# Kernel optimization log

Hardware: AMD Instinct MI355X
Metric: run time of the kernel (lower is better)

The kernel has to match this reference:

```python
import jax, jax.numpy as jnp
import numpy as np

B, INDIM, ENC, BOT, DEC = 2048, 20000, 512, 128, 512
EPS = 1e-5


def _bn(x, g, b):
    # BatchNorm1d in training mode: biased batch stats
    m = jnp.mean(x, axis=0)
    v = jnp.mean(jnp.square(x - m), axis=0)
    return (x - m) * jax.lax.rsqrt(v + EPS) * g + b


def setup_inputs() -> dict:
    key = jax.random.key(0)
    ks = jax.random.split(key, 8)
    s = 0.02  # small init scale keeps exp() outputs finite
    return {
        "x": jax.random.uniform(ks[0], (B, INDIM), dtype=jnp.float32),
        "bn0_g": jnp.ones((INDIM,), jnp.float32),
        "bn0_b": jnp.zeros((INDIM,), jnp.float32),
        "enc_W": jax.random.normal(ks[1], (ENC, INDIM), jnp.float32) * s,
        "enc_b": jnp.zeros((ENC,), jnp.float32),
        "bn1_g": jnp.ones((ENC,), jnp.float32),
        "bn1_b": jnp.zeros((ENC,), jnp.float32),
        "bot_W": jax.random.normal(ks[2], (BOT, ENC), jnp.float32) * s,
        "bot_b": jnp.zeros((BOT,), jnp.float32),
        "bn2_g": jnp.ones((BOT,), jnp.float32),
        "bn2_b": jnp.zeros((BOT,), jnp.float32),
        "dec_W": jax.random.normal(ks[3], (DEC, BOT), jnp.float32) * s,
        "dec_b": jnp.zeros((DEC,), jnp.float32),
        "o1_W": jax.random.normal(ks[4], (INDIM, DEC), jnp.float32) * s,
        "o1_b": jnp.zeros((INDIM,), jnp.float32),
        "o2_W": jax.random.normal(ks[5], (INDIM, DEC), jnp.float32) * s,
        "o2_b": jnp.zeros((INDIM,), jnp.float32),
        "o3_W": jax.random.normal(ks[6], (INDIM, DEC), jnp.float32) * s,
        "o3_b": jnp.zeros((INDIM,), jnp.float32),
    }


def reference(x, bn0_g, bn0_b, enc_W, enc_b, bn1_g, bn1_b, bot_W, bot_b,
              bn2_g, bn2_b, dec_W, dec_b, o1_W, o1_b, o2_W, o2_b, o3_W, o3_b):
    # row-sum / median normalization; diag-inverse @ x == x / s[:, None]
    row_sum = jnp.sum(x, axis=1)                     # [B]
    s = row_sum / jnp.median(row_sum)                # [B]
    h = jnp.log1p(x / s[:, None])                    # log(inv(diag(s)) @ x + 1)
    h = _bn(h, bn0_g, bn0_b)
    h = jax.nn.relu(h @ enc_W.T + enc_b)
    h = _bn(h, bn1_g, bn1_b)
    h = jax.nn.relu(h @ bot_W.T + bot_b)
    h = _bn(h, bn2_g, bn2_b)
    h = jax.nn.relu(h @ dec_W.T + dec_b)
    M = jnp.exp(h @ o1_W.T + o1_b)
    M_loss = s[:, None] * M                          # diag(s) @ M
    pai = jax.nn.sigmoid(h @ o2_W.T + o2_b)
    theta = jnp.exp(h @ o3_W.T + o3_b)
    return pai, M, theta, M_loss
```

## Files before the change

### kernel.cpp

```cpp
#include <hip/hip_runtime.h>
#include <hip/hip_bf16.h>
#include <math.h>

#define B_    2048
#define IND   20000
#define ENCN  512
#define BOTN  128
#define DECN  512
#define KP1   20480
#define NP    20224
#define SPLITK 16
#define KSTEP1 20
#define SPLITK2 4
#define BNEPS 1e-5f

typedef __hip_bfloat16 bf16;
typedef __bf16 bf16x8 __attribute__((ext_vector_type(8)));
typedef float f32x4 __attribute__((ext_vector_type(4)));
typedef unsigned short u16;

__device__ __forceinline__ u16 f2bfu(float f) {
  __hip_bfloat16 h = __float2bfloat16(f);
  return *reinterpret_cast<u16*>(&h);
}

__device__ __forceinline__ void st_b64_bf16(void* p, f32x4 v) {
  union { u16 u[4]; uint2 d; } o;
  o.u[0] = f2bfu(v[0]); o.u[1] = f2bfu(v[1]);
  o.u[2] = f2bfu(v[2]); o.u[3] = f2bfu(v[3]);
  *(uint2*)p = o.d;
}

__device__ __forceinline__ void gload_lds16(const bf16* g, bf16* l) {
  __builtin_amdgcn_global_load_lds(
      (const __attribute__((address_space(1))) void*)g,
      (__attribute__((address_space(3))) void*)l, 16, 0, 0);
}

__global__ void rowsum_k(const float* __restrict__ x, float* __restrict__ row_sum) {
  const int row = blockIdx.x;
  const f32x4* xr = (const f32x4*)(x + (size_t)row * IND);
  float s = 0.f;
  for (int i = threadIdx.x; i < IND / 4; i += 256) {
    f32x4 v = xr[i];
    s += (v[0] + v[1]) + (v[2] + v[3]);
  }
#pragma unroll
  for (int o = 32; o > 0; o >>= 1) s += __shfl_down(s, o, 64);
  __shared__ float ws4[4];
  if ((threadIdx.x & 63) == 0) ws4[threadIdx.x >> 6] = s;
  __syncthreads();
  if (threadIdx.x == 0) row_sum[row] = (ws4[0] + ws4[1]) + (ws4[2] + ws4[3]);
}

__global__ void median_scale_k(const float* __restrict__ row_sum,
                               float* __restrict__ sArr, float* __restrict__ invs) {
  __shared__ float v[B_];
  const int tid = threadIdx.x;
  v[tid] = row_sum[tid];
  v[tid + 1024] = row_sum[tid + 1024];
  __syncthreads();
  for (int k = 2; k <= B_; k <<= 1) {
    for (int j = k >> 1; j > 0; j >>= 1) {
      for (int i = tid; i < B_; i += 1024) {
        int ixj = i ^ j;
        if (ixj > i) {
          bool up = ((i & k) == 0);
          float a = v[i], b = v[ixj];
          if ((a > b) == up) { v[i] = b; v[ixj] = a; }
        }
      }
      __syncthreads();
    }
  }
  float med = 0.5f * (v[B_ / 2 - 1] + v[B_ / 2]);
  for (int i = tid; i < B_; i += 1024) {
    float rs = row_sum[i];
    sArr[i] = rs / med;
    invs[i] = med / rs;
  }
}

__global__ void pass2_k(const float* __restrict__ x, const float* __restrict__ invs,
                        bf16* __restrict__ L, float* __restrict__ part_s,
                        float* __restrict__ part_q) {
  const int c0 = (blockIdx.x * 256 + threadIdx.x) * 4;
  const int rblk = blockIdx.y;
  const int r0 = rblk * 32;
  const bool valid = (c0 < IND);
  f32x4 sum = {0.f, 0.f, 0.f, 0.f}, sq = {0.f, 0.f, 0.f, 0.f};
  for (int r = r0; r < r0 + 32; ++r) {
    f32x4 lv = {0.f, 0.f, 0.f, 0.f};
    if (valid) {
      f32x4 v = *(const f32x4*)(x + (size_t)r * IND + c0);
      float iv = invs[r];
      lv[0] = log1pf(v[0] * iv); lv[1] = log1pf(v[1] * iv);
      lv[2] = log1pf(v[2] * iv); lv[3] = log1pf(v[3] * iv);
      sum += lv; sq += lv * lv;
    }
    ushort4 o;
    o.x = f2bfu(lv[0]); o.y = f2bfu(lv[1]); o.z = f2bfu(lv[2]); o.w = f2bfu(lv[3]);
    *(ushort4*)((u16*)L + (size_t)r * KP1 + c0) = o;
  }
  if (valid) {
    *(f32x4*)(part_s + (size_t)rblk * KP1 + c0) = sum;
    *(f32x4*)(part_q + (size_t)rblk * KP1 + c0) = sq;
  }
}

__global__ void finalize_bn_k(const float* __restrict__ part_s, const float* __restrict__ part_q,
                              const float* __restrict__ g, const float* __restrict__ b,
                              float* __restrict__ scale, float* __restrict__ shift) {
  int c = blockIdx.x * 256 + threadIdx.x;
  if (c >= IND) return;
  float s = 0.f, q = 0.f;
  for (int z = 0; z < 64; ++z) {
    s += part_s[(size_t)z * KP1 + c];
    q += part_q[(size_t)z * KP1 + c];
  }
  const float invN = 1.f / (float)B_;
  float mean = s * invN;
  float var = q * invN - mean * mean;
  float sc = g[c] * rsqrtf(var + BNEPS);
  scale[c] = sc;
  shift[c] = b[c] - mean * sc;
}

__global__ void prepw_k(const float* __restrict__ encW, const float* __restrict__ enc_b,
                        const float* __restrict__ scale0, const float* __restrict__ shift0,
                        bf16* __restrict__ Wp, float* __restrict__ bias1) {
  const int e = blockIdx.x;
  float local = 0.f;
  for (int j0 = threadIdx.x * 4; j0 < KP1; j0 += 1024) {
    ushort4 o;
    if (j0 < IND) {
      f32x4 w = *(const f32x4*)(encW + (size_t)e * IND + j0);
      f32x4 sc = *(const f32x4*)(scale0 + j0);
      f32x4 sh = *(const f32x4*)(shift0 + j0);
      local += sh[0] * w[0] + sh[1] * w[1] + sh[2] * w[2] + sh[3] * w[3];
      o.x = f2bfu(w[0] * sc[0]); o.y = f2bfu(w[1] * sc[1]);
      o.z = f2bfu(w[2] * sc[2]); o.w = f2bfu(w[3] * sc[3]);
    } else {
      o.x = 0; o.y = 0; o.z = 0; o.w = 0;
    }
    *(ushort4*)((u16*)Wp + (size_t)e * KP1 + j0) = o;
  }
#pragma unroll
  for (int o = 32; o > 0; o >>= 1) local += __shfl_down(local, o, 64);
  __shared__ float red[4];
  if ((threadIdx.x & 63) == 0) red[threadIdx.x >> 6] = local;
  __syncthreads();
  if (threadIdx.x == 0) bias1[e] = enc_b[e] + ((red[0] + red[1]) + (red[2] + red[3]));
}

__global__ __launch_bounds__(512, 2)
void gemm1_k(const bf16* __restrict__ A, const bf16* __restrict__ Bm,
             float* __restrict__ Cp) {
  extern __shared__ __align__(16) bf16 smem[];
  bf16* AsB = smem;
  bf16* BsB = smem + 32768;
  const int tid = threadIdx.x;
  const int lane = tid & 63;
  const int wave = tid >> 6;
  const int wr = wave >> 2;
  const int wc = wave & 3;

  const int bid = blockIdx.x;
  const int swz = (bid & 7) * 32 + (bid >> 3);
  const int xm = swz & 7;
  const int rest = swz >> 3;
  const int yn = rest & 1;
  const int z = rest >> 1;
  const int m0 = xm * 256;
  const int n0 = yn * 256;
  const int kbeg = z * KSTEP1 * 64;

  const int srow = tid >> 3;
  const int schunk = (tid & 7) ^ (srow & 7);
  const bf16* gA = A + (size_t)(m0 + srow) * KP1 + kbeg + schunk * 8;
  const bf16* gB = Bm + (size_t)(n0 + srow) * KP1 + kbeg + schunk * 8;
  const int ldst = tid * 8;

  f32x4 acc[8][4] = {};
  const int lrow = lane & 15;
  const int kq = lane >> 4;

  auto STAGE = [&](int ks, int buf) {
    const bf16* ga = gA + (size_t)ks * 64;
    const bf16* gb = gB + (size_t)ks * 64;
    bf16* la = AsB + buf * 16384 + ldst;
    bf16* lb = BsB + buf * 16384 + ldst;
#pragma unroll
    for (int i = 0; i < 4; ++i) {
      gload_lds16(ga + (size_t)(i * 64) * KP1, la + i * 4096);
      gload_lds16(gb + (size_t)(i * 64) * KP1, lb + i * 4096);
    }
  };

  STAGE(0, 0);
  asm volatile("s_waitcnt vmcnt(0)" ::: "memory");
  __builtin_amdgcn_s_barrier();

  int cur = 0;
  for (int ks = 0; ks < KSTEP1; ++ks) {
    if (ks + 1 < KSTEP1) STAGE(ks + 1, cur ^ 1);
    const bf16* As = AsB + cur * 16384;
    const bf16* Bs = BsB + cur * 16384;
#pragma unroll
    for (int kk = 0; kk < 2; ++kk) {
      const int kc = kk * 4 + kq;
      bf16x8 af[8], bfv[4];
#pragma unroll
      for (int m = 0; m < 8; ++m) {
        const int row = wr * 128 + m * 16 + lrow;
        af[m] = *(const bf16x8*)(&As[row * 64 + ((kc ^ (row & 7)) << 3)]);
      }
#pragma unroll
      for (int n = 0; n < 4; ++n) {
        const int row = wc * 64 + n * 16 + lrow;
        bfv[n] = *(const bf16x8*)(&Bs[row * 64 + ((kc ^ (row & 7)) << 3)]);
      }
#pragma unroll
      for (int m = 0; m < 8; ++m)
#pragma unroll
        for (int n = 0; n < 4; ++n)
          acc[m][n] = __builtin_amdgcn_mfma_f32_16x16x32_bf16(bfv[n], af[m], acc[m][n], 0, 0, 0);
    }
    if (ks + 1 < KSTEP1) {
      asm volatile("s_waitcnt vmcnt(0)" ::: "memory");
      __builtin_amdgcn_s_barrier();
      cur ^= 1;
    }
  }

  float* o0 = Cp + (size_t)z * ((size_t)B_ * ENCN);
  const int growb = m0 + wr * 128 + lrow;
  const int gcolb = n0 + wc * 64 + kq * 4;
#pragma unroll
  for (int m = 0; m < 8; ++m) {
    const int grow = growb + m * 16;
#pragma unroll
    for (int n = 0; n < 4; ++n) {
      const int gcol = gcolb + n * 16;
      *(f32x4*)(&o0[(size_t)grow * ENCN + gcol]) = acc[m][n];
    }
  }
}

__global__ __launch_bounds__(512, 2)
void gemm_out_k(const bf16* __restrict__ h3,
                const float* __restrict__ W0, const float* __restrict__ W1,
                const float* __restrict__ W2,
                const float* __restrict__ b0, const float* __restrict__ b1,
                const float* __restrict__ b2,
                const float* __restrict__ sArr, float* __restrict__ out) {
  extern __shared__ __align__(16) bf16 smem[];
  bf16* AsB = smem;
  bf16* BsB = smem + 32768;
  const int tid = threadIdx.x;
  const int lane = tid & 63;
  const int wave = tid >> 6;
  const int wr = wave >> 2;
  const int wc = wave & 3;

  const int bid = blockIdx.x;
  const int swz = (bid & 7) * 237 + (bid >> 3);
  const int g = swz / 632;
  const int r2 = swz - g * 632;
  const int xm = r2 & 7;
  const int yn = r2 >> 3;
  const int m0 = xm * 256;
  const int n0 = yn * 256;

  const float* Wg = (g == 0) ? W0 : (g == 1) ? W1 : W2;
  const float* bg = (g == 0) ? b0 : (g == 1) ? b1 : b2;
  const size_t OFF = (size_t)B_ * IND;
  float* o0 = out + (size_t)g * OFF;
  float* o1 = out + 3 * OFF;

  const int srow = tid >> 3;
  const int schunk = (tid & 7) ^ (srow & 7);
  const bf16* gA = h3 + (size_t)(m0 + srow) * ENCN + schunk * 8;
  const int ldstA = tid * 8;

  const int lrow = lane & 15;
  const int kq = lane >> 4;
  const int bcol = lrow * 4;
  const int brow0 = wave * 32 + kq;

  f32x4 acc[8][4] = {};
  f32x4 bv[8];

  auto LOADA = [&](int ks, int buf) {
    const bf16* ga = gA + ks * 64;
    bf16* la = AsB + buf * 16384 + ldstA;
#pragma unroll
    for (int i = 0; i < 4; ++i)
      gload_lds16(ga + (size_t)(i * 64) * ENCN, la + i * 4096);
  };
  auto LOADB = [&](int ks) {
#pragma unroll
    for (int i = 0; i < 8; ++i) {
      const int gr = n0 + brow0 + i * 4;
      if (gr < IND) bv[i] = *(const f32x4*)(Wg + (size_t)gr * ENCN + ks * 64 + bcol);
      else bv[i] = f32x4{0.f, 0.f, 0.f, 0.f};
    }
  };
  auto WRITEB = [&](int buf) {
    char* lb = (char*)(BsB + buf * 16384);
#pragma unroll
    for (int i = 0; i < 8; ++i) {
      const int r = brow0 + i * 4;
      const int byte = r * 128 + (((lrow >> 1) ^ (r & 7)) << 4) + ((lrow & 1) << 3);
      st_b64_bf16(lb + byte, bv[i]);
    }
  };

  LOADB(0);
  LOADA(0, 0);
  WRITEB(0);
  __syncthreads();

  int cur = 0;
  for (int ks = 0; ks < 8; ++ks) {
    if (ks < 7) { LOADA(ks + 1, cur ^ 1); LOADB(ks + 1); }
    const bf16* As = AsB + cur * 16384;
    const bf16* Bs = BsB + cur * 16384;
#pragma unroll
    for (int kk = 0; kk < 2; ++kk) {
      const int kc = kk * 4 + kq;
      bf16x8 af[8], bfv[4];
#pragma unroll
      for (int m = 0; m < 8; ++m) {
        const int row = wr * 128 + m * 16 + lrow;
        af[m] = *(const bf16x8*)(&As[row * 64 + ((kc ^ (row & 7)) << 3)]);
      }
#pragma unroll
      for (int n = 0; n < 4; ++n) {
        const int row = wc * 64 + n * 16 + lrow;
        bfv[n] = *(const bf16x8*)(&Bs[row * 64 + ((kc ^ (row & 7)) << 3)]);
      }
#pragma unroll
      for (int m = 0; m < 8; ++m)
#pragma unroll
        for (int n = 0; n < 4; ++n)
          acc[m][n] = __builtin_amdgcn_mfma_f32_16x16x32_bf16(bfv[n], af[m], acc[m][n], 0, 0, 0);
    }
    if (ks < 7) {
      WRITEB(cur ^ 1);
      __syncthreads();
      cur ^= 1;
    }
  }

  const int growb = m0 + wr * 128 + lrow;
  const int gcolb = n0 + wc * 64 + kq * 4;
#pragma unroll
  for (int m = 0; m < 8; ++m) {
    const int grow = growb + m * 16;
    float ss = (g == 1) ? sArr[grow] : 0.f;
#pragma unroll
    for (int n = 0; n < 4; ++n) {
      const int gcol = gcolb + n * 16;
      if (gcol < IND) {
        f32x4 t = acc[m][n] + *(const f32x4*)(&bg[gcol]);
        f32x4 r;
        if (g == 0) {
#pragma unroll
          for (int j = 0; j < 4; ++j) r[j] = 1.f / (1.f + __expf(-t[j]));
          *(f32x4*)(&o0[(size_t)grow * IND + gcol]) = r;
        } else {
#pragma unroll
          for (int j = 0; j < 4; ++j) r[j] = __expf(t[j]);
          *(f32x4*)(&o0[(size_t)grow * IND + gcol]) = r;
          if (g == 1) {
            f32x4 rl;
#pragma unroll
            for (int j = 0; j < 4; ++j) rl[j] = ss * r[j];
            *(f32x4*)(&o1[(size_t)grow * IND + gcol]) = rl;
          }
        }
      }
    }
  }
}

template <int EPI>
__global__ __launch_bounds__(256, 2)
void gemm_mid_k(const float* __restrict__ A, int lda,
                const float* __restrict__ scl, const float* __restrict__ sft,
                const float* __restrict__ W, int ldb,
                const float* __restrict__ bias,
                float* __restrict__ outP, bf16* __restrict__ outB, int ldo) {
  __shared__ __align__(16) bf16 As[128 * 64];
  __shared__ __align__(16) bf16 Bs[128 * 64];
  const int tid = threadIdx.x;
  const int lane = tid & 63;
  const int wave = tid >> 6;
  const int wr = wave >> 1, wc = wave & 1;
  const int m0 = blockIdx.x * 128;
  const int n0 = blockIdx.y * 128;
  const int z = blockIdx.z;
  const int kbeg = z * 128;
  const int lrow = lane & 15;
  const int kq = lane >> 4;
  const int scol = lrow * 4;
  const int srow0 = wave * 32 + kq;

  f32x4 acc[4][4] = {};
  for (int ks = 0; ks < 2; ++ks) {
    const int kb = kbeg + ks * 64;
    f32x4 sc4 = *(const f32x4*)(scl + kb + scol);
    f32x4 sf4 = *(const f32x4*)(sft + kb + scol);
#pragma unroll
    for (int i = 0; i < 8; ++i) {
      const int r = srow0 + i * 4;
      const int byte = r * 128 + (((lrow >> 1) ^ (r & 7)) << 4) + ((lrow & 1) << 3);
      f32x4 a = *(const f32x4*)(A + (size_t)(m0 + r) * lda + kb + scol);
      a = a * sc4 + sf4;
      st_b64_bf16((char*)As + byte, a);
      f32x4 b = *(const f32x4*)(W + (size_t)(n0 + r) * ldb + kb + scol);
      st_b64_bf16((char*)Bs + byte, b);
    }
    __syncthreads();
#pragma unroll
    for (int kk = 0; kk < 2; ++kk) {
      const int kc = kk * 4 + kq;
      bf16x8 af[4], bfv[4];
#pragma unroll
      for (int m = 0; m < 4; ++m) {
        const int row = wr * 64 + m * 16 + lrow;
        af[m] = *(const bf16x8*)(&As[row * 64 + ((kc ^ (row & 7)) << 3)]);
      }
#pragma unroll
      for (int n = 0; n < 4; ++n) {
        const int row = wc * 64 + n * 16 + lrow;
        bfv[n] = *(const bf16x8*)(&Bs[row * 64 + ((kc ^ (row & 7)) << 3)]);
      }
#pragma unroll
      for (int m = 0; m < 4; ++m)
#pragma unroll
        for (int n = 0; n < 4; ++n)
          acc[m][n] = __builtin_amdgcn_mfma_f32_16x16x32_bf16(bfv[n], af[m], acc[m][n], 0, 0, 0);
    }
    __syncthreads();
  }

  const int growb = m0 + wr * 64 + lrow;
  const int gcolb = n0 + wc * 64 + kq * 4;
#pragma unroll
  for (int m = 0; m < 4; ++m) {
    const int grow = growb + m * 16;
#pragma unroll
    for (int n = 0; n < 4; ++n) {
      const int gcol = gcolb + n * 16;
      if (EPI == 0) {
        float* op = outP + (size_t)z * ((size_t)B_ * ldo);
        *(f32x4*)(&op[(size_t)grow * ldo + gcol]) = acc[m][n];
      } else {
        f32x4 t = acc[m][n] + *(const f32x4*)(&bias[gcol]);
        f32x4 r;
#pragma unroll
        for (int j = 0; j < 4; ++j) r[j] = fmaxf(t[j], 0.f);
        st_b64_bf16((u16*)outB + (size_t)grow * ldo + gcol, r);
      }
    }
  }
}

__global__ void reduce1c_k(const float* __restrict__ Cp, const float* __restrict__ bias1,
                           float* __restrict__ C1, float* __restrict__ ps,
                           float* __restrict__ pq) {
  const int b = blockIdx.x;
  const int t = threadIdx.x;
  const int c4 = (t & 127) * 4;
  const int rs = t >> 7;
  f32x4 bb = *(const f32x4*)(bias1 + c4);
  f32x4 sum = {0.f, 0.f, 0.f, 0.f}, sq = {0.f, 0.f, 0.f, 0.f};
#pragma unroll
  for (int rr = 0; rr < 4; ++rr) {
    const int row = b * 8 + rs + rr * 2;
    f32x4 v = {0.f, 0.f, 0.f, 0.f};
#pragma unroll
    for (int z = 0; z < SPLITK; ++z)
      v += *(const f32x4*)(Cp + (size_t)z * (B_ * ENCN) + (size_t)row * ENCN + c4);
    v += bb;
    f32x4 r;
#pragma unroll
    for (int j = 0; j < 4; ++j) r[j] = fmaxf(v[j], 0.f);
    *(f32x4*)(C1 + (size_t)row * ENCN + c4) = r;
    sum += r; sq += r * r;
  }
  __shared__ f32x4 ls[2][128], lq[2][128];
  ls[rs][t & 127] = sum; lq[rs][t & 127] = sq;
  __syncthreads();
  if (t < 128) {
    f32x4 s = ls[0][t] + ls[1][t];
    f32x4 q = lq[0][t] + lq[1][t];
    *(f32x4*)(ps + (size_t)b * ENCN + t * 4) = s;
    *(f32x4*)(pq + (size_t)b * ENCN + t * 4) = q;
  }
}

__global__ void reduce2c_k(const float* __restrict__ Cp2, const float* __restrict__ bias,
                           float* __restrict__ C2, float* __restrict__ ps,
                           float* __restrict__ pq) {
  const int b = blockIdx.x;
  const int t = threadIdx.x;
  const int c4 = (t & 31) * 4;
  const int rs = t >> 5;
  f32x4 bb = *(const f32x4*)(bias + c4);
  f32x4 sum = {0.f, 0.f, 0.f, 0.f}, sq = {0.f, 0.f, 0.f, 0.f};
#pragma unroll
  for (int rr = 0; rr < 2; ++rr) {
    const int row = b * 16 + rs + rr * 8;
    f32x4 v = {0.f, 0.f, 0.f, 0.f};
#pragma unroll
    for (int z = 0; z < SPLITK2; ++z)
      v += *(const f32x4*)(Cp2 + (size_t)z * (B_ * BOTN) + (size_t)row * BOTN + c4);
    v += bb;
    f32x4 r;
#pragma unroll
    for (int j = 0; j < 4; ++j) r[j] = fmaxf(v[j], 0.f);
    *(f32x4*)(C2 + (size_t)row * BOTN + c4) = r;
    sum += r; sq += r * r;
  }
  __shared__ f32x4 ls[8][32], lq[8][32];
  ls[rs][t & 31] = sum; lq[rs][t & 31] = sq;
  __syncthreads();
  if (t < 32) {
    f32x4 s = {0.f, 0.f, 0.f, 0.f}, q = {0.f, 0.f, 0.f, 0.f};
#pragma unroll
    for (int k = 0; k < 8; ++k) { s += ls[k][t]; q += lq[k][t]; }
    *(f32x4*)(ps + (size_t)b * BOTN + t * 4) = s;
    *(f32x4*)(pq + (size_t)b * BOTN + t * 4) = q;
  }
}

__global__ void colfin_k(const float* __restrict__ ps, const float* __restrict__ pq,
                         const float* __restrict__ g, const float* __restrict__ b,
                         float* __restrict__ scale, float* __restrict__ shift,
                         int C, int nPart) {
  const int cl = threadIdx.x & 63;
  const int pg = threadIdx.x >> 6;
  const int c = blockIdx.x * 64 + cl;
  float s = 0.f, q = 0.f;
  for (int p = pg; p < nPart; p += 4) {
    s += ps[(size_t)p * C + c];
    q += pq[(size_t)p * C + c];
  }
  __shared__ float ls[4][64], lq[4][64];
  ls[pg][cl] = s; lq[pg][cl] = q;
  __syncthreads();
  if (pg == 0) {
    s = (ls[0][cl] + ls[1][cl]) + (ls[2][cl] + ls[3][cl]);
    q = (lq[0][cl] + lq[1][cl]) + (lq[2][cl] + lq[3][cl]);
    const float invN = 1.f / (float)B_;
    float mean = s * invN;
    float var = q * invN - mean * mean;
    float sc = g[c] * rsqrtf(var + BNEPS);
    scale[c] = sc;
    shift[c] = b[c] - mean * sc;
  }
}

extern "C" void kernel_launch(void* const* d_in, const int* in_sizes, int n_in,
                              void* d_out, int out_size, void* d_ws, size_t ws_size,
                              hipStream_t stream) {
  const float* x     = (const float*)d_in[0];
  const float* bn0_g = (const float*)d_in[1];
  const float* bn0_b = (const float*)d_in[2];
  const float* enc_W = (const float*)d_in[3];
  const float* enc_b = (const float*)d_in[4];
  const float* bn1_g = (const float*)d_in[5];
  const float* bn1_b = (const float*)d_in[6];
  const float* bot_W = (const float*)d_in[7];
  const float* bot_b = (const float*)d_in[8];
  const float* bn2_g = (const float*)d_in[9];
  const float* bn2_b = (const float*)d_in[10];
  const float* dec_W = (const float*)d_in[11];
  const float* dec_b = (const float*)d_in[12];
  const float* o1_W  = (const float*)d_in[13];
  const float* o1_b  = (const float*)d_in[14];
  const float* o2_W  = (const float*)d_in[15];
  const float* o2_b  = (const float*)d_in[16];
  const float* o3_W  = (const float*)d_in[17];
  const float* o3_b  = (const float*)d_in[18];

  char* wsb = (char*)d_ws;
  size_t off = 0;
  auto alloc = [&](size_t bytes) -> void* {
    void* p = wsb + off;
    off = (off + bytes + 255) & ~(size_t)255;
    return p;
  };
  float* row_sum = (float*)alloc(B_ * 4);
  float* sArr    = (float*)alloc(B_ * 4);
  float* invs    = (float*)alloc(B_ * 4);
  float* scale0  = (float*)alloc(IND * 4);
  float* shift0  = (float*)alloc(IND * 4);
  float* bias1   = (float*)alloc(ENCN * 4);
  float* scale1  = (float*)alloc(ENCN * 4);
  float* shift1  = (float*)alloc(ENCN * 4);
  float* scale2  = (float*)alloc(BOTN * 4);
  float* shift2  = (float*)alloc(BOTN * 4);
  float* ps1     = (float*)alloc(256 * ENCN * 4);
  float* pq1     = (float*)alloc(256 * ENCN * 4);
  float* ps2     = (float*)alloc(128 * BOTN * 4);
  float* pq2     = (float*)alloc(128 * BOTN * 4);
  float* C1      = (float*)alloc((size_t)B_ * ENCN * 4);
  float* C2f     = (float*)alloc((size_t)B_ * BOTN * 4);
  float* Cp2     = (float*)alloc((size_t)SPLITK2 * B_ * BOTN * 4);
  float* Cp      = (float*)alloc((size_t)SPLITK * B_ * ENCN * 4);
  bf16*  L       = (bf16*)alloc((size_t)B_ * KP1 * 2);
  bf16*  Wp      = (bf16*)alloc((size_t)ENCN * KP1 * 2);
  bf16*  h3      = (bf16*)alloc((size_t)B_ * DECN * 2);
  float* part_s  = Cp;
  float* part_q  = Cp + (size_t)64 * KP1;

  hipFuncSetAttribute(reinterpret_cast<const void*>(gemm1_k),
                      hipFuncAttributeMaxDynamicSharedMemorySize, 131072);
  hipFuncSetAttribute(reinterpret_cast<const void*>(gemm_out_k),
                      hipFuncAttributeMaxDynamicSharedMemorySize, 131072);

  rowsum_k<<<B_, 256, 0, stream>>>(x, row_sum);
  median_scale_k<<<1, 1024, 0, stream>>>(row_sum, sArr, invs);

  pass2_k<<<dim3(KP1 / 1024, 64), 256, 0, stream>>>(x, invs, L, part_s, part_q);
  finalize_bn_k<<<(IND + 255) / 256, 256, 0, stream>>>(part_s, part_q, bn0_g, bn0_b,
                                                       scale0, shift0);

  prepw_k<<<ENCN, 256, 0, stream>>>(enc_W, enc_b, scale0, shift0, Wp, bias1);

  gemm1_k<<<256, 512, 131072, stream>>>(L, Wp, Cp);
  reduce1c_k<<<256, 256, 0, stream>>>(Cp, bias1, C1, ps1, pq1);
  colfin_k<<<ENCN / 64, 256, 0, stream>>>(ps1, pq1, bn1_g, bn1_b, scale1, shift1,
                                          ENCN, 256);

  gemm_mid_k<0><<<dim3(16, 1, SPLITK2), 256, 0, stream>>>(
      C1, ENCN, scale1, shift1, bot_W, ENCN, nullptr, Cp2, nullptr, BOTN);
  reduce2c_k<<<128, 256, 0, stream>>>(Cp2, bot_b, C2f, ps2, pq2);
  colfin_k<<<BOTN / 64, 256, 0, stream>>>(ps2, pq2, bn2_g, bn2_b, scale2, shift2,
                                          BOTN, 128);
  gemm_mid_k<1><<<dim3(16, 4, 1), 256, 0, stream>>>(
      C2f, BOTN, scale2, shift2, dec_W, BOTN, dec_b, nullptr, h3, DECN);

  float* out = (float*)d_out;
  gemm_out_k<<<1896, 512, 131072, stream>>>(h3, o2_W, o1_W, o3_W,
                                            o2_b, o1_b, o3_b, sArr, out);
}
```

Measured before the change: 728.3 us.

## Restructure GEMM main loops into fine-grained interleaved load/MFMA schedule and pre-convert output weights

Both large GEMMs drop the simple double-buffered loop for a finer schedule. Each 64-wide K tile is split into half-tile global-to-LDS loads issued between small MFMA groups, with partial vmcnt waits, barriers and s_setprio around the MFMA bursts. The row mapping of waves changes to interleave 16-row slices. The output GEMM now reads weights converted once to bf16 by a new kernel, so it can use direct LDS loads instead of fp32 register loads plus conversion. This adds an extra conversion pass over about 60MB of weights each call and many more barriers.

Result: faster. 681.0 us (-6.5%).

```diff
diff --git a/kernel.cpp b/kernel.cpp
--- a/kernel.cpp
+++ b/kernel.cpp
@@ -157,8 +157,8 @@
 void gemm1_k(const bf16* __restrict__ A, const bf16* __restrict__ Bm,
              float* __restrict__ Cp) {
   extern __shared__ __align__(16) bf16 smem[];
-  bf16* AsB = smem;
-  bf16* BsB = smem + 32768;
+  bf16* Asm = smem;
+  bf16* Bsm = smem + 32768;
   const int tid = threadIdx.x;
   const int lane = tid & 63;
   const int wave = tid >> 6;
@@ -179,66 +179,120 @@
   const int schunk = (tid & 7) ^ (srow & 7);
   const bf16* gA = A + (size_t)(m0 + srow) * KP1 + kbeg + schunk * 8;
   const bf16* gB = Bm + (size_t)(n0 + srow) * KP1 + kbeg + schunk * 8;
-  const int ldst = tid * 8;
-
-  f32x4 acc[8][4] = {};
+  const int dst1 = tid * 8;
+
   const int lrow = lane & 15;
   const int kq = lane >> 4;
-
-  auto STAGE = [&](int ks, int buf) {
-    const bf16* ga = gA + (size_t)ks * 64;
-    const bf16* gb = gB + (size_t)ks * 64;
-    bf16* la = AsB + buf * 16384 + ldst;
-    bf16* lb = BsB + buf * 16384 + ldst;
-#pragma unroll
-    for (int i = 0; i < 4; ++i) {
-      gload_lds16(ga + (size_t)(i * 64) * KP1, la + i * 4096);
-      gload_lds16(gb + (size_t)(i * 64) * KP1, lb + i * 4096);
-    }
-  };
-
-  STAGE(0, 0);
-  asm volatile("s_waitcnt vmcnt(0)" ::: "memory");
+  const int rsw = lrow & 7;
+
+  f32x4 acc[8][4] = {};
+  bf16x8 bfv[4][2];
+
+  auto SA = [&](int kt, int half) {
+    const bf16* g = gA + (size_t)(half * 128) * KP1 + (size_t)kt * 64;
+    bf16* l = Asm + (((kt & 1) * 2 + half) << 13) + dst1;
+    gload_lds16(g, l);
+    gload_lds16(g + (size_t)64 * KP1, l + 4096);
+  };
+  auto SB = [&](int kt, int half) {
+    const bf16* g = gB + (size_t)(half * 128) * KP1 + (size_t)kt * 64;
+    bf16* l = Bsm + (((kt & 1) * 2 + half) << 13) + dst1;
+    gload_lds16(g, l);
+    gload_lds16(g + (size_t)64 * KP1, l + 4096);
+  };
+  auto DSA = [&](int slot, int p, bf16x8 af[2][2]) {
+#pragma unroll
+    for (int i = 0; i < 2; ++i) {
+      const int m = 2 * p + i;
+      const int base = ((slot * 2 + (m >> 2)) * 128 + (m & 3) * 32 + wr * 16 + lrow) * 64;
+#pragma unroll
+      for (int kk = 0; kk < 2; ++kk)
+        af[i][kk] = *(const bf16x8*)(&Asm[base + (((kk * 4 + kq) ^ rsw) << 3)]);
+    }
+  };
+  auto DSB = [&](int slot) {
+#pragma unroll
+    for (int n = 0; n < 4; ++n) {
+      const int base = ((slot * 2 + (wc >> 1)) * 128 + (wc & 1) * 64 + n * 16 + lrow) * 64;
+#pragma unroll
+      for (int kk = 0; kk < 2; ++kk)
+        bfv[n][kk] = *(const bf16x8*)(&Bsm[base + (((kk * 4 + kq) ^ rsw) << 3)]);
+    }
+  };
+  auto MF = [&](int p, bf16x8 af[2][2]) {
+    __builtin_amdgcn_s_setprio(1);
+#pragma unroll
+    for (int i = 0; i < 2; ++i)
+#pragma unroll
+      for (int n = 0; n < 4; ++n)
+#pragma unroll
+        for (int kk = 0; kk < 2; ++kk)
+          acc[2 * p + i][n] = __builtin_amdgcn_mfma_f32_16x16x32_bf16(
+              bfv[n][kk], af[i][kk], acc[2 * p + i][n], 0, 0, 0);
+    __builtin_amdgcn_s_setprio(0);
+  };
+
+  SA(0, 0); SA(0, 1); SB(0, 0); SB(0, 1);
+  SB(1, 0); SB(1, 1); SA(1, 0);
+  asm volatile("s_waitcnt vmcnt(6)" ::: "memory");
   __builtin_amdgcn_s_barrier();
 
-  int cur = 0;
-  for (int ks = 0; ks < KSTEP1; ++ks) {
-    if (ks + 1 < KSTEP1) STAGE(ks + 1, cur ^ 1);
-    const bf16* As = AsB + cur * 16384;
-    const bf16* Bs = BsB + cur * 16384;
-#pragma unroll
-    for (int kk = 0; kk < 2; ++kk) {
-      const int kc = kk * 4 + kq;
-      bf16x8 af[8], bfv[4];
-#pragma unroll
-      for (int m = 0; m < 8; ++m) {
-        const int row = wr * 128 + m * 16 + lrow;
-        af[m] = *(const bf16x8*)(&As[row * 64 + ((kc ^ (row & 7)) << 3)]);
-      }
-#pragma unroll
-      for (int n = 0; n < 4; ++n) {
-        const int row = wc * 64 + n * 16 + lrow;
-        bfv[n] = *(const bf16x8*)(&Bs[row * 64 + ((kc ^ (row & 7)) << 3)]);
-      }
-#pragma unroll
-      for (int m = 0; m < 8; ++m)
-#pragma unroll
-        for (int n = 0; n < 4; ++n)
-          acc[m][n] = __builtin_amdgcn_mfma_f32_16x16x32_bf16(bfv[n], af[m], acc[m][n], 0, 0, 0);
-    }
-    if (ks + 1 < KSTEP1) {
-      asm volatile("s_waitcnt vmcnt(0)" ::: "memory");
-      __builtin_amdgcn_s_barrier();
-      cur ^= 1;
-    }
+  const int iters = KSTEP1 >> 1;
+  for (int t = 0; t < iters; ++t) {
+    const int e = 2 * t;
+    const bool last = (t == iters - 1);
+    bf16x8 af[2][2];
+    DSB(0); DSA(0, 0, af);
+    SA(e + 1, 1);
+    __builtin_amdgcn_s_barrier();
+    MF(0, af);
+    __builtin_amdgcn_s_barrier();
+    DSA(0, 1, af);
+    if (!last) SB(e + 2, 0);
+    __builtin_amdgcn_s_barrier();
+    MF(1, af);
+    __builtin_amdgcn_s_barrier();
+    DSA(0, 2, af);
+    if (!last) SB(e + 2, 1);
+    __builtin_amdgcn_s_barrier();
+    MF(2, af);
+    __builtin_amdgcn_s_barrier();
+    DSA(0, 3, af);
+    if (!last) SA(e + 2, 0);
+    if (last) { asm volatile("s_waitcnt vmcnt(0)" ::: "memory"); }
+    else      { asm volatile("s_waitcnt vmcnt(6)" ::: "memory"); }
+    __builtin_amdgcn_s_barrier();
+    MF(3, af);
+    __builtin_amdgcn_s_barrier();
+    DSB(1); DSA(1, 0, af);
+    if (!last) SA(e + 2, 1);
+    __builtin_amdgcn_s_barrier();
+    MF(0, af);
+    __builtin_amdgcn_s_barrier();
+    DSA(1, 1, af);
+    if (!last) SB(e + 3, 0);
+    __builtin_amdgcn_s_barrier();
+    MF(1, af);
+    __builtin_amdgcn_s_barrier();
+    DSA(1, 2, af);
+    if (!last) SB(e + 3, 1);
+    __builtin_amdgcn_s_barrier();
+    MF(2, af);
+    __builtin_amdgcn_s_barrier();
+    DSA(1, 3, af);
+    if (!last) SA(e + 3, 0);
+    if (last) { asm volatile("s_waitcnt vmcnt(0)" ::: "memory"); }
+    else      { asm volatile("s_waitcnt vmcnt(6)" ::: "memory"); }
+    __builtin_amdgcn_s_barrier();
+    MF(3, af);
+    __builtin_amdgcn_s_barrier();
   }
 
   float* o0 = Cp + (size_t)z * ((size_t)B_ * ENCN);
-  const int growb = m0 + wr * 128 + lrow;
   const int gcolb = n0 + wc * 64 + kq * 4;
 #pragma unroll
   for (int m = 0; m < 8; ++m) {
-    const int grow = growb + m * 16;
+    const int grow = m0 + m * 32 + wr * 16 + lrow;
 #pragma unroll
     for (int n = 0; n < 4; ++n) {
       const int gcol = gcolb + n * 16;
@@ -248,15 +302,13 @@
 }
 
 __global__ __launch_bounds__(512, 2)
-void gemm_out_k(const bf16* __restrict__ h3,
-                const float* __restrict__ W0, const float* __restrict__ W1,
-                const float* __restrict__ W2,
+void gemm_out_k(const bf16* __restrict__ A, const bf16* __restrict__ Wall,
                 const float* __restrict__ b0, const float* __restrict__ b1,
                 const float* __restrict__ b2,
                 const float* __restrict__ sArr, float* __restrict__ out) {
   extern __shared__ __align__(16) bf16 smem[];
-  bf16* AsB = smem;
-  bf16* BsB = smem + 32768;
+  bf16* Asm = smem;
+  bf16* Bsm = smem + 32768;
   const int tid = threadIdx.x;
   const int lane = tid & 63;
   const int wave = tid >> 6;
@@ -272,7 +324,7 @@
   const int m0 = xm * 256;
   const int n0 = yn * 256;
 
-  const float* Wg = (g == 0) ? W0 : (g == 1) ? W1 : W2;
+  const bf16* Bm = Wall + (size_t)g * ((size_t)NP * ENCN);
   const float* bg = (g == 0) ? b0 : (g == 1) ? b1 : b2;
   const size_t OFF = (size_t)B_ * IND;
   float* o0 = out + (size_t)g * OFF;
@@ -280,90 +332,129 @@
 
   const int srow = tid >> 3;
   const int schunk = (tid & 7) ^ (srow & 7);
-  const bf16* gA = h3 + (size_t)(m0 + srow) * ENCN + schunk * 8;
-  const int ldstA = tid * 8;
+  const bf16* gA = A + (size_t)(m0 + srow) * ENCN + schunk * 8;
+  const bf16* gB = Bm + (size_t)(n0 + srow) * ENCN + schunk * 8;
+  const int dst1 = tid * 8;
 
   const int lrow = lane & 15;
   const int kq = lane >> 4;
-  const int bcol = lrow * 4;
-  const int brow0 = wave * 32 + kq;
+  const int rsw = lrow & 7;
 
   f32x4 acc[8][4] = {};
-  f32x4 bv[8];
-
-  auto LOADA = [&](int ks, int buf) {
-    const bf16* ga = gA + ks * 64;
-    bf16* la = AsB + buf * 16384 + ldstA;
-#pragma unroll
-    for (int i = 0; i < 4; ++i)
-      gload_lds16(ga + (size_t)(i * 64) * ENCN, la + i * 4096);
-  };
-  auto LOADB = [&](int ks) {
-#pragma unroll
-    for (int i = 0; i < 8; ++i) {
-      const int gr = n0 + brow0 + i * 4;
-      if (gr < IND) bv[i] = *(const f32x4*)(Wg + (size_t)gr * ENCN + ks * 64 + bcol);
-      else bv[i] = f32x4{0.f, 0.f, 0.f, 0.f};
-    }
-  };
-  auto WRITEB = [&](int buf) {
-    char* lb = (char*)(BsB + buf * 16384);
-#pragma unroll
-    for (int i = 0; i < 8; ++i) {
-      const int r = brow0 + i * 4;
-      const int byte = r * 128 + (((lrow >> 1) ^ (r & 7)) << 4) + ((lrow & 1) << 3);
-      st_b64_bf16(lb + byte, bv[i]);
-    }
-  };
-
-  LOADB(0);
-  LOADA(0, 0);
-  WRITEB(0);
-  __syncthreads();
-
-  int cur = 0;
-  for (int ks = 0; ks < 8; ++ks) {
-    if (ks < 7) { LOADA(ks + 1, cur ^ 1); LOADB(ks + 1); }
-    const bf16* As = AsB + cur * 16384;
-    const bf16* Bs = BsB + cur * 16384;
-#pragma unroll
-    for (int kk = 0; kk < 2; ++kk) {
-      const int kc = kk * 4 + kq;
-      bf16x8 af[8], bfv[4];
-#pragma unroll
-      for (int m = 0; m < 8; ++m) {
-        const int row = wr * 128 + m * 16 + lrow;
-        af[m] = *(const bf16x8*)(&As[row * 64 + ((kc ^ (row & 7)) << 3)]);
-      }
-#pragma unroll
-      for (int n = 0; n < 4; ++n) {
-        const int row = wc * 64 + n * 16 + lrow;
-        bfv[n] = *(const bf16x8*)(&Bs[row * 64 + ((kc ^ (row & 7)) << 3)]);
-      }
-#pragma unroll
-      for (int m = 0; m < 8; ++m)
-#pragma unroll
-        for (int n = 0; n < 4; ++n)
-          acc[m][n] = __builtin_amdgcn_mfma_f32_16x16x32_bf16(bfv[n], af[m], acc[m][n], 0, 0, 0);
-    }
-    if (ks < 7) {
-      WRITEB(cur ^ 1);
-      __syncthreads();
-      cur ^= 1;
-    }
-  }
-
-  const int growb = m0 + wr * 128 + lrow;
+  bf16x8 bfv[4][2];
+
+  auto SA = [&](int kt, int half) {
+    const bf16* g_ = gA + (size_t)(half * 128) * ENCN + (size_t)kt * 64;
+    bf16* l = Asm + (((kt & 1) * 2 + half) << 13) + dst1;
+    gload_lds16(g_, l);
+    gload_lds16(g_ + (size_t)64 * ENCN, l + 4096);
+  };
+  auto SB = [&](int kt, int half) {
+    const bf16* g_ = gB + (size_t)(half * 128) * ENCN + (size_t)kt * 64;
+    bf16* l = Bsm + (((kt & 1) * 2 + half) << 13) + dst1;
+    gload_lds16(g_, l);
+    gload_lds16(g_ + (size_t)64 * ENCN, l + 4096);
+  };
+  auto DSA = [&](int slot, int p, bf16x8 af[2][2]) {
+#pragma unroll
+    for (int i = 0; i < 2; ++i) {
+      const int m = 2 * p + i;
+      const int base = ((slot * 2 + (m >> 2)) * 128 + (m & 3) * 32 + wr * 16 + lrow) * 64;
+#pragma unroll
+      for (int kk = 0; kk < 2; ++kk)
+        af[i][kk] = *(const bf16x8*)(&Asm[base + (((kk * 4 + kq) ^ rsw) << 3)]);
+    }
+  };
+  auto DSB = [&](int slot) {
+#pragma unroll
+    for (int n = 0; n < 4; ++n) {
+      const int base = ((slot * 2 + (wc >> 1)) * 128 + (wc & 1) * 64 + n * 16 + lrow) * 64;
+#pragma unroll
+      for (int kk = 0; kk < 2; ++kk)
+        bfv[n][kk] = *(const bf16x8*)(&Bsm[base + (((kk * 4 + kq) ^ rsw) << 3)]);
+    }
+  };
+  auto MF = [&](int p, bf16x8 af[2][2]) {
+    __builtin_amdgcn_s_setprio(1);
+#pragma unroll
+    for (int i = 0; i < 2; ++i)
+#pragma unroll
+      for (int n = 0; n < 4; ++n)
+#pragma unroll
+        for (int kk = 0; kk < 2; ++kk)
+          acc[2 * p + i][n] = __builtin_amdgcn_mfma_f32_16x16x32_bf16(
+              bfv[n][kk], af[i][kk], acc[2 * p + i][n], 0, 0, 0);
+    __builtin_amdgcn_s_setprio(0);
+  };
+
+  SA(0, 0); SA(0, 1); SB(0, 0); SB(0, 1);
+  SB(1, 0); SB(1, 1); SA(1, 0);
+  asm volatile("s_waitcnt vmcnt(6)" ::: "memory");
+  __builtin_amdgcn_s_barrier();
+
+  const int iters = 4;
+  for (int t = 0; t < iters; ++t) {
+    const int e = 2 * t;
+    const bool last = (t == iters - 1);
+    bf16x8 af[2][2];
+    DSB(0); DSA(0, 0, af);
+    SA(e + 1, 1);
+    __builtin_amdgcn_s_barrier();
+    MF(0, af);
+    __builtin_amdgcn_s_barrier();
+    DSA(0, 1, af);
+    if (!last) SB(e + 2, 0);
+    __builtin_amdgcn_s_barrier();
+    MF(1, af);
+    __builtin_amdgcn_s_barrier();
+    DSA(0, 2, af);
+    if (!last) SB(e + 2, 1);
+    __builtin_amdgcn_s_barrier();
+    MF(2, af);
+    __builtin_amdgcn_s_barrier();
+    DSA(0, 3, af);
+    if (!last) SA(e + 2, 0);
+    if (last) { asm volatile("s_waitcnt vmcnt(0)" ::: "memory"); }
+    else      { asm volatile("s_waitcnt vmcnt(6)" ::: "memory"); }
+    __builtin_amdgcn_s_barrier();
+    MF(3, af);
+    __builtin_amdgcn_s_barrier();
+    DSB(1); DSA(1, 0, af);
+    if (!last) SA(e + 2, 1);
+    __builtin_amdgcn_s_barrier();
+    MF(0, af);
+    __builtin_amdgcn_s_barrier();
+    DSA(1, 1, af);
+    if (!last) SB(e + 3, 0);
+    __builtin_amdgcn_s_barrier();
+    MF(1, af);
+    __builtin_amdgcn_s_barrier();
+    DSA(1, 2, af);
+    if (!last) SB(e + 3, 1);
+    __builtin_amdgcn_s_barrier();
+    MF(2, af);
+    __builtin_amdgcn_s_barrier();
+    DSA(1, 3, af);
+    if (!last) SA(e + 3, 0);
+    if (last) { asm volatile("s_waitcnt vmcnt(0)" ::: "memory"); }
+    else      { asm volatile("s_waitcnt vmcnt(6)" ::: "memory"); }
+    __builtin_amdgcn_s_barrier();
+    MF(3, af);
+    __builtin_amdgcn_s_barrier();
+  }
+
   const int gcolb = n0 + wc * 64 + kq * 4;
 #pragma unroll
   for (int m = 0; m < 8; ++m) {
-    const int grow = growb + m * 16;
-    float ss = (g == 1) ? sArr[grow] : 0.f;
+    const int grow = m0 + m * 32 + wr * 16 + lrow;
+    float srow_s = 0.f;
+    if (g == 1) srow_s = sArr[grow];
 #pragma unroll
     for (int n = 0; n < 4; ++n) {
       const int gcol = gcolb + n * 16;
       if (gcol < IND) {
-        f32x4 t = acc[m][n] + *(const f32x4*)(&bg[gcol]);
+        f32x4 bb = *(const f32x4*)(&bg[gcol]);
+        f32x4 t = acc[m][n] + bb;
         f32x4 r;
         if (g == 0) {
 #pragma unroll
@@ -376,7 +467,7 @@
           if (g == 1) {
             f32x4 rl;
 #pragma unroll
-            for (int j = 0; j < 4; ++j) rl[j] = ss * r[j];
+            for (int j = 0; j < 4; ++j) rl[j] = srow_s * r[j];
             *(f32x4*)(&o1[(size_t)grow * IND + gcol]) = rl;
           }
         }
@@ -430,12 +521,12 @@
 #pragma unroll
       for (int m = 0; m < 4; ++m) {
         const int row = wr * 64 + m * 16 + lrow;
-        af[m] = *(const bf16x8*)(&As[row * 64 + ((kc ^ (row & 7)) << 3)]);
+        af[m] = *(const bf16x8*)(&As[row * 64 + (((kc ^ (row & 7)) & 7) << 3)]);
       }
 #pragma unroll
       for (int n = 0; n < 4; ++n) {
         const int row = wc * 64 + n * 16 + lrow;
-        bfv[n] = *(const bf16x8*)(&Bs[row * 64 + ((kc ^ (row & 7)) << 3)]);
+        bfv[n] = *(const bf16x8*)(&Bs[row * 64 + (((kc ^ (row & 7)) & 7) << 3)]);
       }
 #pragma unroll
       for (int m = 0; m < 4; ++m)
@@ -562,6 +653,24 @@
     scale[c] = sc;
     shift[c] = b[c] - mean * sc;
   }
+}
+
+__global__ void cvt_all_k(const float* __restrict__ W0, const float* __restrict__ W1,
+                          const float* __restrict__ W2, bf16* __restrict__ Wb) {
+  const size_t SEG = (size_t)NP * 512;
+  const size_t idx = ((size_t)blockIdx.x * 256 + threadIdx.x) * 4;
+  const int seg = (int)(idx / SEG);
+  const size_t rem = idx - (size_t)seg * SEG;
+  const int e = (int)(rem >> 9);
+  const float* src = (seg == 0) ? W0 : (seg == 1) ? W1 : W2;
+  ushort4 o;
+  if (e < IND) {
+    f32x4 v = *(const f32x4*)(src + rem);
+    o.x = f2bfu(v[0]); o.y = f2bfu(v[1]); o.z = f2bfu(v[2]); o.w = f2bfu(v[3]);
+  } else {
+    o.x = 0; o.y = 0; o.z = 0; o.w = 0;
+  }
+  *(ushort4*)((u16*)Wb + idx) = o;
 }
 
 extern "C" void kernel_launch(void* const* d_in, const int* in_sizes, int n_in,
@@ -615,6 +724,7 @@
   bf16*  L       = (bf16*)alloc((size_t)B_ * KP1 * 2);
   bf16*  Wp      = (bf16*)alloc((size_t)ENCN * KP1 * 2);
   bf16*  h3      = (bf16*)alloc((size_t)B_ * DECN * 2);
+  bf16*  Wall    = (bf16*)alloc((size_t)3 * NP * 512 * 2);
   float* part_s  = Cp;
   float* part_q  = Cp + (size_t)64 * KP1;
 
@@ -645,7 +755,8 @@
   gemm_mid_k<1><<<dim3(16, 4, 1), 256, 0, stream>>>(
       C2f, BOTN, scale2, shift2, dec_W, BOTN, dec_b, nullptr, h3, DECN);
 
+  cvt_all_k<<<(3 * NP * 512) / 1024, 256, 0, stream>>>(o2_W, o1_W, o3_W, Wall);
+
   float* out = (float*)d_out;
-  gemm_out_k<<<1896, 512, 131072, stream>>>(h3, o2_W, o1_W, o3_W,
-                                            o2_b, o1_b, o3_b, sArr, out);
-}
+  gemm_out_k<<<1896, 512, 131072, stream>>>(h3, Wall, o2_b, o1_b, o3_b, sArr, out);
+}
```
